# Performance work log

Measured on AMD Instinct MI355X. Metric: run time of the kernel, lower is better.

Reference implementation:

```python
import jax, jax.numpy as jnp
import numpy as np

N = 100000      # nodes
E = 1600000     # edges
G = 128         # graphs in batch
F_IN = 128
HID = 32
NCLS = 10


def _gcn_conv(x, src, dst, norm, W, b):
    # x: [N, Fin] -> [N, Fout]; src/dst/norm include self-loops: [E+N]
    h = x @ W                                   # dense transform first (Fout=32 < Fin)
    msg = h[src] * norm[:, None]                # gather + edge normalization
    out = jax.ops.segment_sum(msg, dst, num_segments=N)  # scatter-add
    return out + b


def setup_inputs() -> dict:
    key = jax.random.key(0)
    ks = jax.random.split(key, 10)
    x = jax.random.normal(ks[0], (N, F_IN), dtype=jnp.float32)
    edge_index = jax.random.randint(ks[1], (2, E), 0, N, dtype=jnp.int64)
    batch = jnp.sort(jax.random.randint(ks[2], (N,), 0, G, dtype=jnp.int64))
    s = 1.0 / np.sqrt(F_IN)
    W0 = jax.random.normal(ks[3], (F_IN, HID), dtype=jnp.float32) * s
    b0 = jnp.zeros((HID,), dtype=jnp.float32)
    sh = 1.0 / np.sqrt(HID)
    W1 = jax.random.normal(ks[4], (HID, HID), dtype=jnp.float32) * sh
    b1 = jnp.zeros((HID,), dtype=jnp.float32)
    W2 = jax.random.normal(ks[5], (HID, HID), dtype=jnp.float32) * sh
    b2 = jnp.zeros((HID,), dtype=jnp.float32)
    Wl = jax.random.normal(ks[6], (HID, NCLS), dtype=jnp.float32) * sh
    bl = jnp.zeros((NCLS,), dtype=jnp.float32)
    return {"x": x, "edge_index": edge_index, "batch": batch,
            "W0": W0, "b0": b0, "W1": W1, "b1": b1,
            "W2": W2, "b2": b2, "Wl": Wl, "bl": bl}


def reference(x, edge_index, batch, W0, b0, W1, b1, W2, b2, Wl, bl):
    # Self-loop augmented edge list (PyG GCNConv default: add_self_loops=True)
    loop = jnp.arange(N, dtype=edge_index.dtype)
    src = jnp.concatenate([edge_index[0], loop])    # [E+N]
    dst = jnp.concatenate([edge_index[1], loop])
    # Symmetric normalization D^{-1/2} (A+I) D^{-1/2}
    deg = jax.ops.segment_sum(jnp.ones_like(src, dtype=x.dtype), dst, num_segments=N)
    dinv = jax.lax.rsqrt(deg)                       # deg >= 1 thanks to self-loops
    norm = dinv[src] * dinv[dst]                    # [E+N]

    h = x
    for (W, b) in ((W0, b0), (W1, b1), (W2, b2)):
        h = jax.nn.relu(_gcn_conv(h, src, dst, norm, W, b))

    # global mean pool over graphs
    sums = jax.ops.segment_sum(h, batch, num_segments=G)           # [G, HID]
    cnts = jax.ops.segment_sum(jnp.ones((N,), h.dtype), batch, num_segments=G)
    pooled = sums / jnp.maximum(cnts, 1.0)[:, None]

    logits = jax.nn.relu(pooled @ Wl + bl)
    return jax.nn.log_softmax(logits, axis=1)
```

## Files before the change

kernel.cpp:

```cpp
#include <hip/hip_runtime.h>
#include <hip/hip_bf16.h>

#define NN 100000
#define NE 1600000
#define NG 128
#define FIN 128
#define HID 32
#define NCLS 10

#define EG4 (NE / 4)

#define NSL 32
#define GPS (EG4 / NSL)
#define RS 8
#define SUBN (NN / RS)
#define CSRGRID (RS * NSL)
#define CSR_T 1024

#define SCAN_B 1024
#define NB ((NN + SCAN_B - 1) / SCAN_B)

#define POOL_CHUNK 512
#define POOL_SEG 16
#define POOL_GSPAN 32
#define POOL_GRID ((NN + POOL_CHUNK - 1) / POOL_CHUNK)

#define G0_NODES 64
#define G0_GRID ((NN + G0_NODES - 1) / G0_NODES)
#define XPAD 136

#define AGG_GRID (NN / 4)

typedef int int4v __attribute__((ext_vector_type(4)));
typedef __attribute__((ext_vector_type(8))) short short8;
typedef __attribute__((ext_vector_type(4))) float f32x4;

__device__ inline unsigned short f2bf(float f) {
    unsigned int u = __float_as_uint(f);
    unsigned int r = u + 0x7FFFu + ((u >> 16) & 1u);
    return (unsigned short)(r >> 16);
}
__device__ inline float bf2f(unsigned short v) {
    return __uint_as_float(((unsigned int)v) << 16);
}

__global__ void k_init(float* __restrict__ gsum, float* __restrict__ gcnt) {
    int i = blockIdx.x * blockDim.x + threadIdx.x;
    if (i < NG * HID) gsum[i] = 0.f;
    if (i < NG) gcnt[i] = 0.f;
}

__global__ __launch_bounds__(CSR_T) void k_hist3(const int* __restrict__ dst,
                                                 unsigned char* __restrict__ partial) {
    const int r = blockIdx.x & (RS - 1);
    const int s = blockIdx.x >> 3;
    const int node0 = r * SUBN;
    __shared__ int lcnt[SUBN];
    for (int k = threadIdx.x; k < SUBN; k += CSR_T) lcnt[k] = 0;
    __syncthreads();
    const int g1 = (s + 1) * GPS;
    for (int g = s * GPS + threadIdx.x; g < g1; g += CSR_T) {
        const int4v d = *((const int4v*)dst + g);
        unsigned k;
        k = (unsigned)(d.x - node0); if (k < SUBN) atomicAdd(&lcnt[k], 1);
        k = (unsigned)(d.y - node0); if (k < SUBN) atomicAdd(&lcnt[k], 1);
        k = (unsigned)(d.z - node0); if (k < SUBN) atomicAdd(&lcnt[k], 1);
        k = (unsigned)(d.w - node0); if (k < SUBN) atomicAdd(&lcnt[k], 1);
    }
    __syncthreads();
    for (int k = threadIdx.x; k < SUBN; k += CSR_T)
        partial[s * NN + node0 + k] = (unsigned char)lcnt[k];
}

__global__ void k_scanA(unsigned char* __restrict__ partial, int* __restrict__ row_ptr,
                        int* __restrict__ bsum, float* __restrict__ dinv) {
    __shared__ int lds[SCAN_B];
    int i = blockIdx.x * SCAN_B + threadIdx.x;
    int v = 0;
    if (i < NN) {
        int run = 0;
#pragma unroll
        for (int s = 0; s < NSL; s++) {
            int c = partial[s * NN + i];
            partial[s * NN + i] = (unsigned char)run;
            run += c;
        }
        v = run;
        dinv[i] = rsqrtf((float)v + 1.0f);
    }
    lds[threadIdx.x] = v;
    __syncthreads();
    int val = v;
    for (int off = 1; off < SCAN_B; off <<= 1) {
        int u = 0;
        if ((int)threadIdx.x >= off) u = lds[threadIdx.x - off];
        __syncthreads();
        if ((int)threadIdx.x >= off) { val += u; lds[threadIdx.x] = val; }
        __syncthreads();
    }
    if (i < NN) row_ptr[i] = val - v;
    if (threadIdx.x == SCAN_B - 1) bsum[blockIdx.x] = val;
}

__global__ void k_scanB(int* __restrict__ bsum) {
    __shared__ int lds[128];
    int t = threadIdx.x;
    int v = (t < NB) ? bsum[t] : 0;
    lds[t] = v;
    __syncthreads();
    int val = v;
    for (int off = 1; off < 128; off <<= 1) {
        int u = 0;
        if (t >= off) u = lds[t - off];
        __syncthreads();
        if (t >= off) { val += u; lds[t] = val; }
        __syncthreads();
    }
    if (t < NB) bsum[t] = val - v;
}

__global__ void k_scanC(int* __restrict__ row_ptr, const int* __restrict__ bsum) {
    int i = blockIdx.x * SCAN_B + threadIdx.x;
    if (i < NN) row_ptr[i] += bsum[blockIdx.x];
    if (i == 0) row_ptr[NN] = NE;
}

__global__ __launch_bounds__(CSR_T) void k_scat3(const int* __restrict__ src,
                                                 const int* __restrict__ dst,
                                                 const int* __restrict__ row_ptr,
                                                 const unsigned char* __restrict__ pref,
                                                 int* __restrict__ csr_src) {
    const int r = blockIdx.x & (RS - 1);
    const int s = blockIdx.x >> 3;
    const int node0 = r * SUBN;
    __shared__ int lcur[SUBN];
    for (int k = threadIdx.x; k < SUBN; k += CSR_T)
        lcur[k] = row_ptr[node0 + k] + (int)pref[s * NN + node0 + k];
    __syncthreads();
    const int g1 = (s + 1) * GPS;
    for (int g = s * GPS + threadIdx.x; g < g1; g += CSR_T) {
        const int4v d = *((const int4v*)dst + g);
        const int4v sx = *((const int4v*)src + g);
        unsigned k;
        k = (unsigned)(d.x - node0); if (k < SUBN) { int p = atomicAdd(&lcur[k], 1); csr_src[p] = sx.x; }
        k = (unsigned)(d.y - node0); if (k < SUBN) { int p = atomicAdd(&lcur[k], 1); csr_src[p] = sx.y; }
        k = (unsigned)(d.z - node0); if (k < SUBN) { int p = atomicAdd(&lcur[k], 1); csr_src[p] = sx.z; }
        k = (unsigned)(d.w - node0); if (k < SUBN) { int p = atomicAdd(&lcur[k], 1); csr_src[p] = sx.w; }
    }
}

__global__ void k_gemm0(const float* __restrict__ x, const float* __restrict__ W,
                        const float* __restrict__ dinv, unsigned short* __restrict__ t) {
    __shared__ __align__(16) unsigned short x_lds[G0_NODES][XPAD];
    __shared__ __align__(16) unsigned short wt_lds[HID][XPAD];
    const int tid = threadIdx.x;
    const int node0 = blockIdx.x * G0_NODES;

#pragma unroll
    for (int r = 0; r < 8; r++) {
        int q = tid + 256 * r;
        int row = q >> 5;
        int c4 = q & 31;
        float4 xv = {0.f, 0.f, 0.f, 0.f};
        int node = node0 + row;
        if (node < NN) xv = ((const float4*)(x + (size_t)node * FIN))[c4];
        ushort4 b;
        b.x = f2bf(xv.x); b.y = f2bf(xv.y); b.z = f2bf(xv.z); b.w = f2bf(xv.w);
        *(ushort4*)&x_lds[row][c4 * 4] = b;
    }
#pragma unroll
    for (int r = 0; r < 16; r++) {
        int q = tid + 256 * r;
        int k = q >> 5, n = q & 31;
        wt_lds[n][k] = f2bf(W[q]);
    }
    __syncthreads();

    const int w = tid >> 6;
    const int lane = tid & 63;
    const int row = lane & 15;
    const int kg = lane >> 4;
    const int w16 = w * 16;

    f32x4 acc0 = {0.f, 0.f, 0.f, 0.f};
    f32x4 acc1 = {0.f, 0.f, 0.f, 0.f};
#pragma unroll
    for (int s = 0; s < 4; s++) {
        short8 a  = *(const short8*)&x_lds[w16 + row][s * 32 + kg * 8];
        short8 b0 = *(const short8*)&wt_lds[row][s * 32 + kg * 8];
        short8 b1 = *(const short8*)&wt_lds[16 + row][s * 32 + kg * 8];
        acc0 = __builtin_amdgcn_mfma_f32_16x16x32_bf16(a, b0, acc0, 0, 0, 0);
        acc1 = __builtin_amdgcn_mfma_f32_16x16x32_bf16(a, b1, acc1, 0, 0, 0);
    }

    const int f = lane & 15;
#pragma unroll
    for (int j = 0; j < 4; j++) {
        int node = node0 + w16 + kg * 4 + j;
        if (node < NN) {
            float di = dinv[node];
            t[(size_t)node * HID + f]      = f2bf(acc0[j] * di);
            t[(size_t)node * HID + 16 + f] = f2bf(acc1[j] * di);
        }
    }
}

__global__ void k_gemmh(const unsigned short* __restrict__ h, const float* __restrict__ W,
                        const float* __restrict__ dinv, unsigned short* __restrict__ t) {
    __shared__ float Ws[HID * HID];
    for (int j = threadIdx.x; j < HID * HID; j += 256) Ws[j] = W[j];
    __syncthreads();
    int gid = blockIdx.x * 256 + threadIdx.x;
    int i = gid >> 5, f = gid & 31;
    if (i >= NN) return;
    const short8* hr = (const short8*)(h + (size_t)i * HID);
    float acc = 0.f;
#pragma unroll
    for (int q = 0; q < 4; q++) {
        short8 hv = hr[q];
#pragma unroll
        for (int j = 0; j < 8; j++) {
            int k = q * 8 + j;
            acc = fmaf(bf2f((unsigned short)hv[j]), Ws[k * HID + f], acc);
        }
    }
    t[(size_t)i * HID + f] = f2bf(acc * dinv[i]);
}

__global__ __launch_bounds__(256, 8) void k_agg(const unsigned short* __restrict__ t,
                                                const int* __restrict__ row_ptr,
                                                const int* __restrict__ csr_src,
                                                const float* __restrict__ dinv,
                                                const float* __restrict__ b,
                                                unsigned short* __restrict__ hout) {
    const int wid = (blockIdx.x * 256 + threadIdx.x) >> 6;
    if (wid >= NN) return;
    const int lane = threadIdx.x & 63;
    const int f = lane & 31;
    const int half = lane >> 5;
    const int beg = row_ptr[wid], end = row_ptr[wid + 1];
    float acc = half ? 0.f : bf2f(t[(size_t)wid * HID + f]);
    int e = beg;
    for (; e + 16 <= end; e += 16) {
        int4v ia, ib;
        __builtin_memcpy(&ia, csr_src + e + half * 8, 16);
        __builtin_memcpy(&ib, csr_src + e + half * 8 + 4, 16);
        unsigned short u0 = t[(size_t)ia.x * HID + f];
        unsigned short u1 = t[(size_t)ia.y * HID + f];
        unsigned short u2 = t[(size_t)ia.z * HID + f];
        unsigned short u3 = t[(size_t)ia.w * HID + f];
        unsigned short u4 = t[(size_t)ib.x * HID + f];
        unsigned short u5 = t[(size_t)ib.y * HID + f];
        unsigned short u6 = t[(size_t)ib.z * HID + f];
        unsigned short u7 = t[(size_t)ib.w * HID + f];
        acc += ((bf2f(u0) + bf2f(u1)) + (bf2f(u2) + bf2f(u3)))
             + ((bf2f(u4) + bf2f(u5)) + (bf2f(u6) + bf2f(u7)));
    }
    if (e + 8 <= end) {
        int4v ia;
        __builtin_memcpy(&ia, csr_src + e + half * 4, 16);
        unsigned short u0 = t[(size_t)ia.x * HID + f];
        unsigned short u1 = t[(size_t)ia.y * HID + f];
        unsigned short u2 = t[(size_t)ia.z * HID + f];
        unsigned short u3 = t[(size_t)ia.w * HID + f];
        acc += (bf2f(u0) + bf2f(u1)) + (bf2f(u2) + bf2f(u3));
        e += 8;
    }
    if (e + 4 <= end) {
        int2 ii;
        __builtin_memcpy(&ii, csr_src + e + half * 2, 8);
        unsigned short u0 = t[(size_t)ii.x * HID + f];
        unsigned short u1 = t[(size_t)ii.y * HID + f];
        acc += bf2f(u0) + bf2f(u1);
        e += 4;
    }
    if (e + 2 <= end) {
        int s = csr_src[e + half];
        acc += bf2f(t[(size_t)s * HID + f]);
        e += 2;
    }
    if (e < end && half == 0) {
        acc += bf2f(t[(size_t)csr_src[e] * HID + f]);
    }
    acc += __shfl_xor(acc, 32, 64);
    if (half == 0) {
        float r = fmaf(acc, dinv[wid], b[f]);
        hout[(size_t)wid * HID + f] = f2bf(fmaxf(r, 0.f));
    }
}

__global__ void k_pool2(const unsigned short* __restrict__ h, const int* __restrict__ batch,
                        float* __restrict__ gsum, float* __restrict__ gcnt) {
    __shared__ float lacc[POOL_GSPAN][HID];
    __shared__ float lcnt[POOL_GSPAN];
    __shared__ int s_gmin;
    const int chunk_start = blockIdx.x * POOL_CHUNK;

    for (int j = threadIdx.x; j < POOL_GSPAN * HID; j += 256) ((float*)lacc)[j] = 0.f;
    if (threadIdx.x < POOL_GSPAN) lcnt[threadIdx.x] = 0.f;
    if (threadIdx.x == 0) {
        int cs = chunk_start < NN ? chunk_start : NN - 1;
        s_gmin = batch[cs];
    }
    __syncthreads();
    const int gmin = s_gmin;

    const int seg = threadIdx.x >> 3;
    const int l = (threadIdx.x & 7) * 4;
    const int i0 = chunk_start + seg * POOL_SEG;

    float4 acc = {0.f, 0.f, 0.f, 0.f};
    float cnt = 0.f;
    int cur_g = -1;

    for (int k = 0; k < POOL_SEG; k++) {
        int i = i0 + k;
        if (i >= NN) break;
        int g = batch[i];
        if (g != cur_g) {
            if (cur_g >= 0) {
                int bin = cur_g - gmin;
                if (bin >= 0 && bin < POOL_GSPAN) {
                    atomicAdd(&lacc[bin][l + 0], acc.x);
                    atomicAdd(&lacc[bin][l + 1], acc.y);
                    atomicAdd(&lacc[bin][l + 2], acc.z);
                    atomicAdd(&lacc[bin][l + 3], acc.w);
                    if (l == 0) atomicAdd(&lcnt[bin], cnt);
                } else {
                    atomicAdd(&gsum[cur_g * HID + l + 0], acc.x);
                    atomicAdd(&gsum[cur_g * HID + l + 1], acc.y);
                    atomicAdd(&gsum[cur_g * HID + l + 2], acc.z);
                    atomicAdd(&gsum[cur_g * HID + l + 3], acc.w);
                    if (l == 0) atomicAdd(&gcnt[cur_g], cnt);
                }
            }
            cur_g = g;
            acc.x = acc.y = acc.z = acc.w = 0.f;
            cnt = 0.f;
        }
        const ushort4 v = *(const ushort4*)&h[(size_t)i * HID + l];
        acc.x += bf2f(v.x); acc.y += bf2f(v.y);
        acc.z += bf2f(v.z); acc.w += bf2f(v.w);
        cnt += 1.f;
    }
    if (cur_g >= 0) {
        int bin = cur_g - gmin;
        if (bin >= 0 && bin < POOL_GSPAN) {
            atomicAdd(&lacc[bin][l + 0], acc.x);
            atomicAdd(&lacc[bin][l + 1], acc.y);
            atomicAdd(&lacc[bin][l + 2], acc.z);
            atomicAdd(&lacc[bin][l + 3], acc.w);
            if (l == 0) atomicAdd(&lcnt[bin], cnt);
        } else {
            atomicAdd(&gsum[cur_g * HID + l + 0], acc.x);
            atomicAdd(&gsum[cur_g * HID + l + 1], acc.y);
            atomicAdd(&gsum[cur_g * HID + l + 2], acc.z);
            atomicAdd(&gsum[cur_g * HID + l + 3], acc.w);
            if (l == 0) atomicAdd(&gcnt[cur_g], cnt);
        }
    }
    __syncthreads();

    for (int j = threadIdx.x; j < POOL_GSPAN * HID; j += 256) {
        int bin = j / HID, f = j % HID;
        int g = gmin + bin;
        float v = lacc[bin][f];
        if (g < NG && v != 0.f) atomicAdd(&gsum[g * HID + f], v);
    }
    if (threadIdx.x < POOL_GSPAN) {
        int g = gmin + threadIdx.x;
        float c = lcnt[threadIdx.x];
        if (g < NG && c != 0.f) atomicAdd(&gcnt[g], c);
    }
}

__global__ void k_classify(const float* __restrict__ gsum, const float* __restrict__ gcnt,
                           const float* __restrict__ Wl, const float* __restrict__ bl,
                           float* __restrict__ out) {
    __shared__ float w[HID * NCLS];
    __shared__ float bb[NCLS];
    int t = threadIdx.x;
    for (int j = t; j < HID * NCLS; j += blockDim.x) w[j] = Wl[j];
    if (t < NCLS) bb[t] = bl[t];
    __syncthreads();
    if (t >= NG) return;
    float c = gcnt[t];
    c = c > 1.f ? c : 1.f;
    float p[HID];
#pragma unroll
    for (int k = 0; k < HID; k++) p[k] = gsum[t * HID + k] / c;
    float lg[NCLS];
    float m = -1e30f;
#pragma unroll
    for (int c2 = 0; c2 < NCLS; c2++) {
        float a = bb[c2];
#pragma unroll
        for (int k = 0; k < HID; k++) a = fmaf(p[k], w[k * NCLS + c2], a);
        a = a > 0.f ? a : 0.f;
        lg[c2] = a;
        m = fmaxf(m, a);
    }
    float s = 0.f;
#pragma unroll
    for (int c2 = 0; c2 < NCLS; c2++) s += expf(lg[c2] - m);
    float ls = logf(s);
#pragma unroll
    for (int c2 = 0; c2 < NCLS; c2++) out[t * NCLS + c2] = lg[c2] - m - ls;
}

extern "C" void kernel_launch(void* const* d_in, const int* in_sizes, int n_in,
                              void* d_out, int out_size, void* d_ws, size_t ws_size,
                              hipStream_t stream) {
    const float* x  = (const float*)d_in[0];
    const int* ei   = (const int*)d_in[1];
    const int* batch = (const int*)d_in[2];
    const float* W0 = (const float*)d_in[3];
    const float* b0 = (const float*)d_in[4];
    const float* W1 = (const float*)d_in[5];
    const float* b1 = (const float*)d_in[6];
    const float* W2 = (const float*)d_in[7];
    const float* b2 = (const float*)d_in[8];
    const float* Wl = (const float*)d_in[9];
    const float* bl = (const float*)d_in[10];
    float* out = (float*)d_out;

    const int* esrc = ei;
    const int* edst = ei + NE;

    char* ws = (char*)d_ws;
    size_t off = 0;
    auto alloc = [&](size_t bytes) -> void* {
        void* p = ws + off;
        off = (off + bytes + 511) & ~(size_t)511;
        return p;
    };
    int*   row_ptr = (int*)alloc((NN + 1) * sizeof(int));
    float* dinv    = (float*)alloc(NN * sizeof(float));
    int*   bsum    = (int*)alloc(256 * sizeof(int));
    int*   csr_src = (int*)alloc(NE * sizeof(int));
    unsigned short* tbuf = (unsigned short*)alloc((size_t)NN * HID * sizeof(unsigned short));
    unsigned short* hA   = (unsigned short*)alloc((size_t)NN * HID * sizeof(unsigned short));
    unsigned short* hB   = (unsigned short*)alloc((size_t)NN * HID * sizeof(unsigned short));
    float* gsum    = (float*)alloc(NG * HID * sizeof(float));
    float* gcnt    = (float*)alloc(NG * sizeof(float));
    (void)ws_size; (void)in_sizes; (void)n_in; (void)out_size;

    unsigned char* partial = (unsigned char*)tbuf;

    k_init<<<17, 256, 0, stream>>>(gsum, gcnt);
    k_hist3<<<CSRGRID, CSR_T, 0, stream>>>(edst, partial);
    k_scanA<<<NB, SCAN_B, 0, stream>>>(partial, row_ptr, bsum, dinv);
    k_scanB<<<1, 128, 0, stream>>>(bsum);
    k_scanC<<<NB, SCAN_B, 0, stream>>>(row_ptr, bsum);
    k_scat3<<<CSRGRID, CSR_T, 0, stream>>>(esrc, edst, row_ptr, partial, csr_src);

    const int gemm_grid = (NN * HID + 255) / 256;

    k_gemm0<<<G0_GRID, 256, 0, stream>>>(x, W0, dinv, tbuf);
    k_agg<<<AGG_GRID, 256, 0, stream>>>(tbuf, row_ptr, csr_src, dinv, b0, hA);
    k_gemmh<<<gemm_grid, 256, 0, stream>>>(hA, W1, dinv, tbuf);
    k_agg<<<AGG_GRID, 256, 0, stream>>>(tbuf, row_ptr, csr_src, dinv, b1, hB);
    k_gemmh<<<gemm_grid, 256, 0, stream>>>(hB, W2, dinv, tbuf);
    k_agg<<<AGG_GRID, 256, 0, stream>>>(tbuf, row_ptr, csr_src, dinv, b2, hA);

    k_pool2<<<POOL_GRID, 256, 0, stream>>>(hA, batch, gsum, gcnt);
    k_classify<<<1, 128, 0, stream>>>(gsum, gcnt, Wl, bl, out);
}
```

Measured before the change: 245.2 us.

## Pad CSR rows to multiples of 16 with a zero dummy node to drop agg tail code

```diff
diff --git a/kernel.cpp b/kernel.cpp
--- a/kernel.cpp
+++ b/kernel.cpp
@@ -17,6 +17,9 @@
 #define CSRGRID (RS * NSL)
 #define CSR_T 1024
 
+#define PAD 16
+#define NEP (NE + NN * PAD)
+
 #define SCAN_B 1024
 #define NB ((NN + SCAN_B - 1) / SCAN_B)
 
@@ -44,10 +47,12 @@
     return __uint_as_float(((unsigned int)v) << 16);
 }
 
-__global__ void k_init(float* __restrict__ gsum, float* __restrict__ gcnt) {
+__global__ void k_init(float* __restrict__ gsum, float* __restrict__ gcnt,
+                       unsigned short* __restrict__ tzero) {
     int i = blockIdx.x * blockDim.x + threadIdx.x;
     if (i < NG * HID) gsum[i] = 0.f;
     if (i < NG) gcnt[i] = 0.f;
+    if (i < HID) tzero[i] = 0;
 }
 
 __global__ __launch_bounds__(CSR_T) void k_hist3(const int* __restrict__ dst,
@@ -73,10 +78,11 @@
 }
 
 __global__ void k_scanA(unsigned char* __restrict__ partial, int* __restrict__ row_ptr,
-                        int* __restrict__ bsum, float* __restrict__ dinv) {
+                        int* __restrict__ bsum, float* __restrict__ dinv,
+                        int* __restrict__ deg) {
     __shared__ int lds[SCAN_B];
     int i = blockIdx.x * SCAN_B + threadIdx.x;
-    int v = 0;
+    int pv = 0;
     if (i < NN) {
         int run = 0;
 #pragma unroll
@@ -85,12 +91,13 @@
             partial[s * NN + i] = (unsigned char)run;
             run += c;
         }
-        v = run;
-        dinv[i] = rsqrtf((float)v + 1.0f);
-    }
-    lds[threadIdx.x] = v;
-    __syncthreads();
-    int val = v;
+        deg[i] = run;
+        dinv[i] = rsqrtf((float)run + 1.0f);
+        pv = (run + PAD - 1) & ~(PAD - 1);
+    }
+    lds[threadIdx.x] = pv;
+    __syncthreads();
+    int val = pv;
     for (int off = 1; off < SCAN_B; off <<= 1) {
         int u = 0;
         if ((int)threadIdx.x >= off) u = lds[threadIdx.x - off];
@@ -98,7 +105,7 @@
         if ((int)threadIdx.x >= off) { val += u; lds[threadIdx.x] = val; }
         __syncthreads();
     }
-    if (i < NN) row_ptr[i] = val - v;
+    if (i < NN) row_ptr[i] = val - pv;
     if (threadIdx.x == SCAN_B - 1) bsum[blockIdx.x] = val;
 }
 
@@ -119,10 +126,25 @@
     if (t < NB) bsum[t] = val - v;
 }
 
-__global__ void k_scanC(int* __restrict__ row_ptr, const int* __restrict__ bsum) {
+__global__ void k_scanC(int* __restrict__ row_ptr, const int* __restrict__ bsum,
+                        const int* __restrict__ deg) {
     int i = blockIdx.x * SCAN_B + threadIdx.x;
-    if (i < NN) row_ptr[i] += bsum[blockIdx.x];
-    if (i == 0) row_ptr[NN] = NE;
+    if (i < NN) {
+        int r = row_ptr[i] + bsum[blockIdx.x];
+        row_ptr[i] = r;
+        if (i == NN - 1)
+            row_ptr[NN] = r + ((deg[i] + PAD - 1) & ~(PAD - 1));
+    }
+}
+
+__global__ void k_pad(const int* __restrict__ row_ptr, const int* __restrict__ deg,
+                      int* __restrict__ csr_src) {
+    int i = blockIdx.x * blockDim.x + threadIdx.x;
+    if (i >= NN) return;
+    int start = row_ptr[i];
+    int d = deg[i];
+    int pd = (d + PAD - 1) & ~(PAD - 1);
+    for (int j = start + d; j < start + pd; j++) csr_src[j] = NN;
 }
 
 __global__ __launch_bounds__(CSR_T) void k_scat3(const int* __restrict__ src,
@@ -240,11 +262,9 @@
     const int half = lane >> 5;
     const int beg = row_ptr[wid], end = row_ptr[wid + 1];
     float acc = half ? 0.f : bf2f(t[(size_t)wid * HID + f]);
-    int e = beg;
-    for (; e + 16 <= end; e += 16) {
-        int4v ia, ib;
-        __builtin_memcpy(&ia, csr_src + e + half * 8, 16);
-        __builtin_memcpy(&ib, csr_src + e + half * 8 + 4, 16);
+    for (int e = beg; e < end; e += 16) {
+        const int4v ia = *(const int4v*)(csr_src + e + half * 8);
+        const int4v ib = *(const int4v*)(csr_src + e + half * 8 + 4);
         unsigned short u0 = t[(size_t)ia.x * HID + f];
         unsigned short u1 = t[(size_t)ia.y * HID + f];
         unsigned short u2 = t[(size_t)ia.z * HID + f];
@@ -255,32 +275,6 @@
         unsigned short u7 = t[(size_t)ib.w * HID + f];
         acc += ((bf2f(u0) + bf2f(u1)) + (bf2f(u2) + bf2f(u3)))
              + ((bf2f(u4) + bf2f(u5)) + (bf2f(u6) + bf2f(u7)));
-    }
-    if (e + 8 <= end) {
-        int4v ia;
-        __builtin_memcpy(&ia, csr_src + e + half * 4, 16);
-        unsigned short u0 = t[(size_t)ia.x * HID + f];
-        unsigned short u1 = t[(size_t)ia.y * HID + f];
-        unsigned short u2 = t[(size_t)ia.z * HID + f];
-        unsigned short u3 = t[(size_t)ia.w * HID + f];
-        acc += (bf2f(u0) + bf2f(u1)) + (bf2f(u2) + bf2f(u3));
-        e += 8;
-    }
-    if (e + 4 <= end) {
-        int2 ii;
-        __builtin_memcpy(&ii, csr_src + e + half * 2, 8);
-        unsigned short u0 = t[(size_t)ii.x * HID + f];
-        unsigned short u1 = t[(size_t)ii.y * HID + f];
-        acc += bf2f(u0) + bf2f(u1);
-        e += 4;
-    }
-    if (e + 2 <= end) {
-        int s = csr_src[e + half];
-        acc += bf2f(t[(size_t)s * HID + f]);
-        e += 2;
-    }
-    if (e < end && half == 0) {
-        acc += bf2f(t[(size_t)csr_src[e] * HID + f]);
     }
     acc += __shfl_xor(acc, 32, 64);
     if (half == 0) {
@@ -436,9 +430,10 @@
     };
     int*   row_ptr = (int*)alloc((NN + 1) * sizeof(int));
     float* dinv    = (float*)alloc(NN * sizeof(float));
+    int*   deg     = (int*)alloc(NN * sizeof(int));
     int*   bsum    = (int*)alloc(256 * sizeof(int));
-    int*   csr_src = (int*)alloc(NE * sizeof(int));
-    unsigned short* tbuf = (unsigned short*)alloc((size_t)NN * HID * sizeof(unsigned short));
+    int*   csr_src = (int*)alloc((size_t)NEP * sizeof(int));
+    unsigned short* tbuf = (unsigned short*)alloc((size_t)(NN + 1) * HID * sizeof(unsigned short));
     unsigned short* hA   = (unsigned short*)alloc((size_t)NN * HID * sizeof(unsigned short));
     unsigned short* hB   = (unsigned short*)alloc((size_t)NN * HID * sizeof(unsigned short));
     float* gsum    = (float*)alloc(NG * HID * sizeof(float));
@@ -446,12 +441,14 @@
     (void)ws_size; (void)in_sizes; (void)n_in; (void)out_size;
 
     unsigned char* partial = (unsigned char*)tbuf;
-
-    k_init<<<17, 256, 0, stream>>>(gsum, gcnt);
+    unsigned short* tzero = tbuf + (size_t)NN * HID;
+
+    k_init<<<17, 256, 0, stream>>>(gsum, gcnt, tzero);
     k_hist3<<<CSRGRID, CSR_T, 0, stream>>>(edst, partial);
-    k_scanA<<<NB, SCAN_B, 0, stream>>>(partial, row_ptr, bsum, dinv);
+    k_scanA<<<NB, SCAN_B, 0, stream>>>(partial, row_ptr, bsum, dinv, deg);
     k_scanB<<<1, 128, 0, stream>>>(bsum);
-    k_scanC<<<NB, SCAN_B, 0, stream>>>(row_ptr, bsum);
+    k_scanC<<<NB, SCAN_B, 0, stream>>>(row_ptr, bsum, deg);
+    k_pad<<<(NN + 255) / 256, 256, 0, stream>>>(row_ptr, deg, csr_src);
     k_scat3<<<CSRGRID, CSR_T, 0, stream>>>(esrc, edst, row_ptr, partial, csr_src);
 
     const int gemm_grid = (NN * HID + 255) / 256;
```

After: 230.1 us. -6.2%, faster.
